# Performance work log

Hardware: AMD Instinct MI355X
Metric: run time of the kernel (lower is better)

Reference implementation:

```python
import jax, jax.numpy as jnp
import numpy as np

NEG_INF = 1e10  # module's self.inf


def setup_inputs() -> dict:
    key = jax.random.key(0)
    k1, k2, k3, k4 = jax.random.split(key, 4)
    B, To, Ti, d = 16, 2048, 2048, 64
    q = jax.random.normal(k1, (B, To, d), dtype=jnp.float32)
    k = jax.random.normal(k2, (B, Ti, d), dtype=jnp.float32)
    v = jax.random.normal(k3, (B, Ti, d), dtype=jnp.float32)
    prod_mask = jax.random.randint(k4, (B, To, Ti), 0, 2, dtype=jnp.int32)
    return {"q": q, "k": k, "v": v, "prod_mask": prod_mask}


def reference(q, k, v, prod_mask):
    d_qk = q.shape[2]
    # [B, To, Ti] scores
    scaled_qk = jnp.einsum('bod,bid->boi', q, k) / jnp.sqrt(jnp.float32(d_qk))
    scaled_qk = jnp.where(prod_mask == 0, jnp.float32(-NEG_INF), scaled_qk)
    weights = jax.nn.softmax(scaled_qk, axis=2)
    # v flattened over trailing dims is already [B, Ti, d] here
    attended_v = jnp.einsum('boi,bid->bod', weights, v)
    return attended_v
```

## Files before the change

kernel.cpp:

```cpp
#include <hip/hip_runtime.h>
#include <stdint.h>

#define BATCH 16
#define TO 2048
#define TI 2048
#define DH 64
#define NITER (TI / 64)

typedef __attribute__((ext_vector_type(8))) short bf16x8;
typedef __attribute__((ext_vector_type(4))) float f32x4;

__device__ __forceinline__ unsigned short f2bf(float f) {
  uint32_t x = __float_as_uint(f);
  x += 0x7fffu + ((x >> 16) & 1u);
  return (unsigned short)(x >> 16);
}

__global__ __launch_bounds__(256) void convert_kv(
    const float* __restrict__ kg, const float* __restrict__ vg,
    unsigned short* __restrict__ k_bf, unsigned short* __restrict__ v_t) {
  __shared__ __align__(16) unsigned short vt[64][72];
  int b = blockIdx.y;
  int i0 = blockIdx.x * 64;
  int t = threadIdx.x;

  {
    const float4* src = (const float4*)(kg + ((size_t)b * TI + i0) * DH);
    ushort4* dst = (ushort4*)(k_bf + ((size_t)b * TI + i0) * DH);
#pragma unroll
    for (int u = 0; u < 4; ++u) {
      float4 f = src[t + 256 * u];
      ushort4 o;
      o.x = f2bf(f.x); o.y = f2bf(f.y); o.z = f2bf(f.z); o.w = f2bf(f.w);
      dst[t + 256 * u] = o;
    }
  }
  {
    const float4* src = (const float4*)(vg + ((size_t)b * TI + i0) * DH);
#pragma unroll
    for (int u = 0; u < 4; ++u) {
      int idx = t + 256 * u;
      int row = idx >> 4;
      int c4 = idx & 15;
      float4 f = src[idx];
      vt[c4 * 4 + 0][row] = f2bf(f.x);
      vt[c4 * 4 + 1][row] = f2bf(f.y);
      vt[c4 * 4 + 2][row] = f2bf(f.z);
      vt[c4 * 4 + 3][row] = f2bf(f.w);
    }
  }
  __syncthreads();
  {
    int dd = t >> 2, part = t & 3;
    ushort4* dst = (ushort4*)(v_t + ((size_t)b * DH + dd) * TI + i0 + part * 16);
#pragma unroll
    for (int u = 0; u < 4; ++u) {
      ushort4 o;
      o.x = vt[dd][part * 16 + u * 4 + 0];
      o.y = vt[dd][part * 16 + u * 4 + 1];
      o.z = vt[dd][part * 16 + u * 4 + 2];
      o.w = vt[dd][part * 16 + u * 4 + 3];
      dst[u] = o;
    }
  }
}

#define ATTN_BODY(CUR, IC, MCUR, MNXT)                                         \
  {                                                                            \
    if ((IC) < NITER - 1) {                                                    \
      _Pragma("unroll") for (int mt = 0; mt < 4; ++mt)                         \
          MNXT[mt] = *(const int4*)(mbase + mt * 16);                          \
      mbase += 64;                                                             \
         \
      *(uint4*)&k_lds[(CUR) ^ 1][row][part * 16] = ka0;                        \
      *(uint4*)&k_lds[(CUR) ^ 1][row][part * 16 + 8] = ka1;                    \
      *(uint4*)&v_lds[(CUR) ^ 1][row][part * 16] = va0;                        \
      *(uint4*)&v_lds[(CUR) ^ 1][row][part * 16 + 8] = va1;                    \
    }                                                                          \
        \
    if ((IC) < NITER - 2) {                                                    \
      ka0 = kp[0]; ka1 = kp[1];                                                \
      va0 = vp[0]; va1 = vp[1];                                                \
      kp = (const uint4*)((const char*)kp + 64 * DH * 2);                      \
      vp = (const uint4*)((const char*)vp + 64 * 2);                           \
    }                                                                          \
                                                  \
    f32x4 st[4];                                                               \
    _Pragma("unroll") for (int mt = 0; mt < 4; ++mt) {                         \
      bf16x8 kf0 = *(const bf16x8*)&k_lds[CUR][mt * 16 + ln15][quad * 8];      \
      bf16x8 kf1 = *(const bf16x8*)&k_lds[CUR][mt * 16 + ln15][32 + quad * 8]; \
      f32x4 acc = (f32x4){0.f, 0.f, 0.f, 0.f};                                 \
      acc = __builtin_amdgcn_mfma_f32_16x16x32_bf16(kf0, qf[0], acc, 0, 0, 0); \
      acc = __builtin_amdgcn_mfma_f32_16x16x32_bf16(kf1, qf[1], acc, 0, 0, 0); \
      st[mt] = acc;                                                            \
    }                                                                          \
         \
    _Pragma("unroll") for (int mt = 0; mt < 4; ++mt) {                         \
      float p0 = (MCUR[mt].x != 0) ? __expf(st[mt][0]) : 0.f;                  \
      float p1 = (MCUR[mt].y != 0) ? __expf(st[mt][1]) : 0.f;                  \
      float p2 = (MCUR[mt].z != 0) ? __expf(st[mt][2]) : 0.f;                  \
      float p3 = (MCUR[mt].w != 0) ? __expf(st[mt][3]) : 0.f;                  \
      l_part += (p0 + p1) + (p2 + p3);                                         \
      uint32_t lo = (uint32_t)f2bf(p0) | ((uint32_t)f2bf(p1) << 16);           \
      uint32_t hi = (uint32_t)f2bf(p2) | ((uint32_t)f2bf(p3) << 16);           \
      uint2 pk; pk.x = lo; pk.y = hi;                                          \
      *(uint2*)&p_row[wave][ln15][mt * 16 + quad * 4] = pk;                    \
    }                                                                          \
            \
    bf16x8 pf0 = *(const bf16x8*)&p_row[wave][ln15][quad * 8];                 \
    bf16x8 pf1 = *(const bf16x8*)&p_row[wave][ln15][32 + quad * 8];            \
                                             \
    _Pragma("unroll") for (int dt = 0; dt < 4; ++dt) {                         \
      bf16x8 vf0 = *(const bf16x8*)&v_lds[CUR][dt * 16 + ln15][quad * 8];      \
      bf16x8 vf1 = *(const bf16x8*)&v_lds[CUR][dt * 16 + ln15][32 + quad * 8]; \
      o_acc[dt] = __builtin_amdgcn_mfma_f32_16x16x32_bf16(vf0, pf0, o_acc[dt], 0, 0, 0); \
      o_acc[dt] = __builtin_amdgcn_mfma_f32_16x16x32_bf16(vf1, pf1, o_acc[dt], 0, 0, 0); \
    }                                                                          \
          \
    asm volatile("s_waitcnt lgkmcnt(0)\n\ts_barrier" ::: "memory");            \
  }

__global__ __launch_bounds__(256) void attn_kernel(
    const float* __restrict__ q, const int* __restrict__ mask,
    const unsigned short* __restrict__ k_bf, const unsigned short* __restrict__ v_t,
    float* __restrict__ out) {
  __shared__ __align__(16) unsigned short k_lds[2][64][72];
  __shared__ __align__(16) unsigned short v_lds[2][64][72];
  __shared__ __align__(16) unsigned short p_row[4][16][72];

  int n = blockIdx.x;
  int xcd = n & 7;
  int slot = n >> 3;
  int b = (xcd << 1) | (slot >> 5);
  int o_blk = slot & 31;

  int t = threadIdx.x;
  int wave = t >> 6;
  int lane = t & 63;
  int ln15 = lane & 15;
  int quad = lane >> 4;

  int o0 = o_blk * 64 + wave * 16;
  int qrow = o0 + ln15;

  bf16x8 qf[2];
  {
    const float* qp = q + ((size_t)b * TO + qrow) * DH;
#pragma unroll
    for (int kc = 0; kc < 2; ++kc) {
      int kk = kc * 32 + quad * 8;
      float4 f0 = *(const float4*)(qp + kk);
      float4 f1 = *(const float4*)(qp + kk + 4);
      bf16x8 a;
      a[0] = (short)f2bf(f0.x * 0.125f);
      a[1] = (short)f2bf(f0.y * 0.125f);
      a[2] = (short)f2bf(f0.z * 0.125f);
      a[3] = (short)f2bf(f0.w * 0.125f);
      a[4] = (short)f2bf(f1.x * 0.125f);
      a[5] = (short)f2bf(f1.y * 0.125f);
      a[6] = (short)f2bf(f1.z * 0.125f);
      a[7] = (short)f2bf(f1.w * 0.125f);
      qf[kc] = a;
    }
  }

  f32x4 o_acc[4];
#pragma unroll
  for (int dt = 0; dt < 4; ++dt) o_acc[dt] = (f32x4){0.f, 0.f, 0.f, 0.f};
  float l_part = 0.f;

  int row = t >> 2, part = t & 3;
  const uint4* kp = (const uint4*)(k_bf + ((size_t)b * TI + row) * DH + part * 16);
  const uint4* vp = (const uint4*)(v_t + ((size_t)b * DH + row) * TI + part * 16);
  const int* mbase = mask + ((size_t)b * TO + qrow) * TI + quad * 4;

  uint4 ka0 = kp[0], ka1 = kp[1];
  uint4 va0 = vp[0], va1 = vp[1];
  kp = (const uint4*)((const char*)kp + 64 * DH * 2);
  vp = (const uint4*)((const char*)vp + 64 * 2);
  *(uint4*)&k_lds[0][row][part * 16] = ka0;
  *(uint4*)&k_lds[0][row][part * 16 + 8] = ka1;
  *(uint4*)&v_lds[0][row][part * 16] = va0;
  *(uint4*)&v_lds[0][row][part * 16 + 8] = va1;
  ka0 = kp[0]; ka1 = kp[1];
  va0 = vp[0]; va1 = vp[1];
  kp = (const uint4*)((const char*)kp + 64 * DH * 2);
  vp = (const uint4*)((const char*)vp + 64 * 2);
  int4 mv[4], mw[4];
#pragma unroll
  for (int mt = 0; mt < 4; ++mt) mv[mt] = *(const int4*)(mbase + mt * 16);
  mbase += 64;
  asm volatile("s_waitcnt lgkmcnt(0)\n\ts_barrier" ::: "memory");

  for (int ic = 0; ic < NITER; ic += 2) {
    ATTN_BODY(0, ic, mv, mw)
    ATTN_BODY(1, ic + 1, mw, mv)
  }

  l_part += __shfl_xor(l_part, 16);
  l_part += __shfl_xor(l_part, 32);
  float inv = 1.0f / l_part;
  float* orow = out + ((size_t)b * TO + qrow) * DH;
#pragma unroll
  for (int dt = 0; dt < 4; ++dt) {
    float4 vout;
    vout.x = o_acc[dt][0] * inv;
    vout.y = o_acc[dt][1] * inv;
    vout.z = o_acc[dt][2] * inv;
    vout.w = o_acc[dt][3] * inv;
    *(float4*)(orow + dt * 16 + quad * 4) = vout;
  }
}

extern "C" void kernel_launch(void* const* d_in, const int* in_sizes, int n_in,
                              void* d_out, int out_size, void* d_ws, size_t ws_size,
                              hipStream_t stream) {
  const float* q = (const float*)d_in[0];
  const float* k = (const float*)d_in[1];
  const float* v = (const float*)d_in[2];
  const int* mask = (const int*)d_in[3];

  unsigned short* k_bf = (unsigned short*)d_ws;
  unsigned short* v_t = k_bf + (size_t)BATCH * TI * DH;

  convert_kv<<<dim3(TI / 64, BATCH), 256, 0, stream>>>(k, v, k_bf, v_t);
  attn_kernel<<<dim3(TO / 64 * BATCH), 256, 0, stream>>>(q, mask, k_bf, v_t, (float*)d_out);
}
```

Measured before the change: 77.57 us.

## Load K and V MFMA fragments directly from global memory, drop LDS staging

```diff
diff --git a/kernel.cpp b/kernel.cpp
--- a/kernel.cpp
+++ b/kernel.cpp
@@ -65,33 +65,27 @@
   }
 }
 
-#define ATTN_BODY(CUR, IC, MCUR, MNXT)                                         \
+#define ATTN_BODY(IC, MCUR, MNXT)                                              \
   {                                                                            \
     if ((IC) < NITER - 1) {                                                    \
       _Pragma("unroll") for (int mt = 0; mt < 4; ++mt)                         \
           MNXT[mt] = *(const int4*)(mbase + mt * 16);                          \
       mbase += 64;                                                             \
-         \
-      *(uint4*)&k_lds[(CUR) ^ 1][row][part * 16] = ka0;                        \
-      *(uint4*)&k_lds[(CUR) ^ 1][row][part * 16 + 8] = ka1;                    \
-      *(uint4*)&v_lds[(CUR) ^ 1][row][part * 16] = va0;                        \
-      *(uint4*)&v_lds[(CUR) ^ 1][row][part * 16 + 8] = va1;                    \
-    }                                                                          \
-        \
-    if ((IC) < NITER - 2) {                                                    \
-      ka0 = kp[0]; ka1 = kp[1];                                                \
-      va0 = vp[0]; va1 = vp[1];                                                \
-      kp = (const uint4*)((const char*)kp + 64 * DH * 2);                      \
-      vp = (const uint4*)((const char*)vp + 64 * 2);                           \
-    }                                                                          \
-                                                  \
+    }                                                                          \
+                              \
+    const unsigned short* kc = k_base + (size_t)(IC) * 64 * DH;                \
+    bf16x8 kf[8];                                                              \
+    _Pragma("unroll") for (int mt = 0; mt < 4; ++mt) {                         \
+      const unsigned short* kr = kc + (mt * 16 + ln15) * DH + quad * 8;        \
+      kf[2 * mt] = *(const bf16x8*)kr;                                         \
+      kf[2 * mt + 1] = *(const bf16x8*)(kr + 32);                              \
+    }                                                                          \
+                                                              \
     f32x4 st[4];                                                               \
     _Pragma("unroll") for (int mt = 0; mt < 4; ++mt) {                         \
-      bf16x8 kf0 = *(const bf16x8*)&k_lds[CUR][mt * 16 + ln15][quad * 8];      \
-      bf16x8 kf1 = *(const bf16x8*)&k_lds[CUR][mt * 16 + ln15][32 + quad * 8]; \
       f32x4 acc = (f32x4){0.f, 0.f, 0.f, 0.f};                                 \
-      acc = __builtin_amdgcn_mfma_f32_16x16x32_bf16(kf0, qf[0], acc, 0, 0, 0); \
-      acc = __builtin_amdgcn_mfma_f32_16x16x32_bf16(kf1, qf[1], acc, 0, 0, 0); \
+      acc = __builtin_amdgcn_mfma_f32_16x16x32_bf16(kf[2 * mt], qf[0], acc, 0, 0, 0);     \
+      acc = __builtin_amdgcn_mfma_f32_16x16x32_bf16(kf[2 * mt + 1], qf[1], acc, 0, 0, 0); \
       st[mt] = acc;                                                            \
     }                                                                          \
          \
@@ -109,23 +103,21 @@
             \
     bf16x8 pf0 = *(const bf16x8*)&p_row[wave][ln15][quad * 8];                 \
     bf16x8 pf1 = *(const bf16x8*)&p_row[wave][ln15][32 + quad * 8];            \
-                                             \
+                     \
+    const unsigned short* vc = v_base + (size_t)(IC) * 64;                     \
     _Pragma("unroll") for (int dt = 0; dt < 4; ++dt) {                         \
-      bf16x8 vf0 = *(const bf16x8*)&v_lds[CUR][dt * 16 + ln15][quad * 8];      \
-      bf16x8 vf1 = *(const bf16x8*)&v_lds[CUR][dt * 16 + ln15][32 + quad * 8]; \
+      const unsigned short* vr = vc + (size_t)(dt * 16 + ln15) * TI + quad * 8;\
+      bf16x8 vf0 = *(const bf16x8*)vr;                                         \
+      bf16x8 vf1 = *(const bf16x8*)(vr + 32);                                  \
       o_acc[dt] = __builtin_amdgcn_mfma_f32_16x16x32_bf16(vf0, pf0, o_acc[dt], 0, 0, 0); \
       o_acc[dt] = __builtin_amdgcn_mfma_f32_16x16x32_bf16(vf1, pf1, o_acc[dt], 0, 0, 0); \
     }                                                                          \
-          \
-    asm volatile("s_waitcnt lgkmcnt(0)\n\ts_barrier" ::: "memory");            \
   }
 
 __global__ __launch_bounds__(256) void attn_kernel(
     const float* __restrict__ q, const int* __restrict__ mask,
     const unsigned short* __restrict__ k_bf, const unsigned short* __restrict__ v_t,
     float* __restrict__ out) {
-  __shared__ __align__(16) unsigned short k_lds[2][64][72];
-  __shared__ __align__(16) unsigned short v_lds[2][64][72];
   __shared__ __align__(16) unsigned short p_row[4][16][72];
 
   int n = blockIdx.x;
@@ -169,32 +161,18 @@
   for (int dt = 0; dt < 4; ++dt) o_acc[dt] = (f32x4){0.f, 0.f, 0.f, 0.f};
   float l_part = 0.f;
 
-  int row = t >> 2, part = t & 3;
-  const uint4* kp = (const uint4*)(k_bf + ((size_t)b * TI + row) * DH + part * 16);
-  const uint4* vp = (const uint4*)(v_t + ((size_t)b * DH + row) * TI + part * 16);
+  const unsigned short* k_base = k_bf + (size_t)b * TI * DH;
+  const unsigned short* v_base = v_t + (size_t)b * DH * TI;
   const int* mbase = mask + ((size_t)b * TO + qrow) * TI + quad * 4;
 
-  uint4 ka0 = kp[0], ka1 = kp[1];
-  uint4 va0 = vp[0], va1 = vp[1];
-  kp = (const uint4*)((const char*)kp + 64 * DH * 2);
-  vp = (const uint4*)((const char*)vp + 64 * 2);
-  *(uint4*)&k_lds[0][row][part * 16] = ka0;
-  *(uint4*)&k_lds[0][row][part * 16 + 8] = ka1;
-  *(uint4*)&v_lds[0][row][part * 16] = va0;
-  *(uint4*)&v_lds[0][row][part * 16 + 8] = va1;
-  ka0 = kp[0]; ka1 = kp[1];
-  va0 = vp[0]; va1 = vp[1];
-  kp = (const uint4*)((const char*)kp + 64 * DH * 2);
-  vp = (const uint4*)((const char*)vp + 64 * 2);
   int4 mv[4], mw[4];
 #pragma unroll
   for (int mt = 0; mt < 4; ++mt) mv[mt] = *(const int4*)(mbase + mt * 16);
   mbase += 64;
-  asm volatile("s_waitcnt lgkmcnt(0)\n\ts_barrier" ::: "memory");
 
   for (int ic = 0; ic < NITER; ic += 2) {
-    ATTN_BODY(0, ic, mv, mw)
-    ATTN_BODY(1, ic + 1, mw, mv)
+    ATTN_BODY(ic, mv, mw)
+    ATTN_BODY(ic + 1, mw, mv)
   }
 
   l_part += __shfl_xor(l_part, 16);
```

Result: slower. 159.9 us (+106.1%).

## Split key dimension across two wave groups per block with LDS reduction

Applied to the files above, without the earlier changes.

```diff
diff --git a/kernel.cpp b/kernel.cpp
--- a/kernel.cpp
+++ b/kernel.cpp
@@ -5,7 +5,7 @@
 #define TO 2048
 #define TI 2048
 #define DH 64
-#define NITER (TI / 64)
+#define NITER2 16
 
 typedef __attribute__((ext_vector_type(8))) short bf16x8;
 typedef __attribute__((ext_vector_type(4))) float f32x4;
@@ -65,30 +65,18 @@
   }
 }
 
-#define ATTN_BODY(CUR, IC, MCUR, MNXT)                                         \
+#define ATTN_BODY(IC, MCUR, MNXT)                                              \
   {                                                                            \
-    if ((IC) < NITER - 1) {                                                    \
+    if ((IC) < NITER2 - 1) {                                                   \
       _Pragma("unroll") for (int mt = 0; mt < 4; ++mt)                         \
           MNXT[mt] = *(const int4*)(mbase + mt * 16);                          \
       mbase += 64;                                                             \
-         \
-      *(uint4*)&k_lds[(CUR) ^ 1][row][part * 16] = ka0;                        \
-      *(uint4*)&k_lds[(CUR) ^ 1][row][part * 16 + 8] = ka1;                    \
-      *(uint4*)&v_lds[(CUR) ^ 1][row][part * 16] = va0;                        \
-      *(uint4*)&v_lds[(CUR) ^ 1][row][part * 16 + 8] = va1;                    \
-    }                                                                          \
-        \
-    if ((IC) < NITER - 2) {                                                    \
-      ka0 = kp[0]; ka1 = kp[1];                                                \
-      va0 = vp[0]; va1 = vp[1];                                                \
-      kp = (const uint4*)((const char*)kp + 64 * DH * 2);                      \
-      vp = (const uint4*)((const char*)vp + 64 * 2);                           \
-    }                                                                          \
-                                                  \
+    }                                                                          \
+                                        \
     f32x4 st[4];                                                               \
     _Pragma("unroll") for (int mt = 0; mt < 4; ++mt) {                         \
-      bf16x8 kf0 = *(const bf16x8*)&k_lds[CUR][mt * 16 + ln15][quad * 8];      \
-      bf16x8 kf1 = *(const bf16x8*)&k_lds[CUR][mt * 16 + ln15][32 + quad * 8]; \
+      bf16x8 kf0 = *(const bf16x8*)&k_lds[g][mt * 16 + ln15][quad * 8];        \
+      bf16x8 kf1 = *(const bf16x8*)&k_lds[g][mt * 16 + ln15][32 + quad * 8];   \
       f32x4 acc = (f32x4){0.f, 0.f, 0.f, 0.f};                                 \
       acc = __builtin_amdgcn_mfma_f32_16x16x32_bf16(kf0, qf[0], acc, 0, 0, 0); \
       acc = __builtin_amdgcn_mfma_f32_16x16x32_bf16(kf1, qf[1], acc, 0, 0, 0); \
@@ -109,24 +97,40 @@
             \
     bf16x8 pf0 = *(const bf16x8*)&p_row[wave][ln15][quad * 8];                 \
     bf16x8 pf1 = *(const bf16x8*)&p_row[wave][ln15][32 + quad * 8];            \
-                                             \
+                                                         \
     _Pragma("unroll") for (int dt = 0; dt < 4; ++dt) {                         \
-      bf16x8 vf0 = *(const bf16x8*)&v_lds[CUR][dt * 16 + ln15][quad * 8];      \
-      bf16x8 vf1 = *(const bf16x8*)&v_lds[CUR][dt * 16 + ln15][32 + quad * 8]; \
+      bf16x8 vf0 = *(const bf16x8*)&v_lds[g][dt * 16 + ln15][quad * 8];        \
+      bf16x8 vf1 = *(const bf16x8*)&v_lds[g][dt * 16 + ln15][32 + quad * 8];   \
       o_acc[dt] = __builtin_amdgcn_mfma_f32_16x16x32_bf16(vf0, pf0, o_acc[dt], 0, 0, 0); \
       o_acc[dt] = __builtin_amdgcn_mfma_f32_16x16x32_bf16(vf1, pf1, o_acc[dt], 0, 0, 0); \
     }                                                                          \
-          \
+                                          \
     asm volatile("s_waitcnt lgkmcnt(0)\n\ts_barrier" ::: "memory");            \
-  }
-
-__global__ __launch_bounds__(256) void attn_kernel(
+    if ((IC) < NITER2 - 1) {                                                   \
+                        \
+      *(uint4*)&k_lds[g][row][part * 16] = ka0;                                \
+      *(uint4*)&k_lds[g][row][part * 16 + 8] = ka1;                            \
+      *(uint4*)&v_lds[g][row][part * 16] = va0;                                \
+      *(uint4*)&v_lds[g][row][part * 16 + 8] = va1;                            \
+               \
+      if ((IC) < NITER2 - 2) {                                                 \
+        ka0 = kp[0]; ka1 = kp[1];                                              \
+        va0 = vp[0]; va1 = vp[1];                                              \
+        kp = (const uint4*)((const char*)kp + 64 * DH * 2);                    \
+        vp = (const uint4*)((const char*)vp + 64 * 2);                         \
+      }                                                                        \
+                                    \
+      asm volatile("s_waitcnt lgkmcnt(0)\n\ts_barrier" ::: "memory");          \
+    }                                                                          \
+  }
+
+__global__ __launch_bounds__(512) void attn_kernel(
     const float* __restrict__ q, const int* __restrict__ mask,
     const unsigned short* __restrict__ k_bf, const unsigned short* __restrict__ v_t,
     float* __restrict__ out) {
   __shared__ __align__(16) unsigned short k_lds[2][64][72];
   __shared__ __align__(16) unsigned short v_lds[2][64][72];
-  __shared__ __align__(16) unsigned short p_row[4][16][72];
+  __shared__ __align__(16) unsigned short p_row[8][16][72];
 
   int n = blockIdx.x;
   int xcd = n & 7;
@@ -136,12 +140,13 @@
 
   int t = threadIdx.x;
   int wave = t >> 6;
+  int g = wave >> 2;
+  int w = wave & 3;
   int lane = t & 63;
   int ln15 = lane & 15;
   int quad = lane >> 4;
 
-  int o0 = o_blk * 64 + wave * 16;
-  int qrow = o0 + ln15;
+  int qrow = o_blk * 64 + w * 16 + ln15;
 
   bf16x8 qf[2];
   {
@@ -169,19 +174,20 @@
   for (int dt = 0; dt < 4; ++dt) o_acc[dt] = (f32x4){0.f, 0.f, 0.f, 0.f};
   float l_part = 0.f;
 
-  int row = t >> 2, part = t & 3;
-  const uint4* kp = (const uint4*)(k_bf + ((size_t)b * TI + row) * DH + part * 16);
-  const uint4* vp = (const uint4*)(v_t + ((size_t)b * DH + row) * TI + part * 16);
-  const int* mbase = mask + ((size_t)b * TO + qrow) * TI + quad * 4;
+  int tg = t & 255;
+  int row = tg >> 2, part = tg & 3;
+  const uint4* kp = (const uint4*)(k_bf + ((size_t)b * TI + g * 1024 + row) * DH + part * 16);
+  const uint4* vp = (const uint4*)(v_t + ((size_t)b * DH + row) * TI + g * 1024 + part * 16);
+  const int* mbase = mask + ((size_t)b * TO + qrow) * TI + g * 1024 + quad * 4;
 
   uint4 ka0 = kp[0], ka1 = kp[1];
   uint4 va0 = vp[0], va1 = vp[1];
   kp = (const uint4*)((const char*)kp + 64 * DH * 2);
   vp = (const uint4*)((const char*)vp + 64 * 2);
-  *(uint4*)&k_lds[0][row][part * 16] = ka0;
-  *(uint4*)&k_lds[0][row][part * 16 + 8] = ka1;
-  *(uint4*)&v_lds[0][row][part * 16] = va0;
-  *(uint4*)&v_lds[0][row][part * 16 + 8] = va1;
+  *(uint4*)&k_lds[g][row][part * 16] = ka0;
+  *(uint4*)&k_lds[g][row][part * 16 + 8] = ka1;
+  *(uint4*)&v_lds[g][row][part * 16] = va0;
+  *(uint4*)&v_lds[g][row][part * 16 + 8] = va1;
   ka0 = kp[0]; ka1 = kp[1];
   va0 = vp[0]; va1 = vp[1];
   kp = (const uint4*)((const char*)kp + 64 * DH * 2);
@@ -192,23 +198,38 @@
   mbase += 64;
   asm volatile("s_waitcnt lgkmcnt(0)\n\ts_barrier" ::: "memory");
 
-  for (int ic = 0; ic < NITER; ic += 2) {
-    ATTN_BODY(0, ic, mv, mw)
-    ATTN_BODY(1, ic + 1, mw, mv)
+  for (int ic = 0; ic < NITER2; ic += 2) {
+    ATTN_BODY(ic, mv, mw)
+    ATTN_BODY(ic + 1, mw, mv)
   }
 
   l_part += __shfl_xor(l_part, 16);
   l_part += __shfl_xor(l_part, 32);
-  float inv = 1.0f / l_part;
-  float* orow = out + ((size_t)b * TO + qrow) * DH;
-#pragma unroll
-  for (int dt = 0; dt < 4; ++dt) {
-    float4 vout;
-    vout.x = o_acc[dt][0] * inv;
-    vout.y = o_acc[dt][1] * inv;
-    vout.z = o_acc[dt][2] * inv;
-    vout.w = o_acc[dt][3] * inv;
-    *(float4*)(orow + dt * 16 + quad * 4) = vout;
+
+  float* scr = (float*)&k_lds[0][0][0];
+  float* lscr = (float*)&p_row[0][0][0];
+  int orow_i = w * 16 + ln15;
+
+  if (g == 1) {
+#pragma unroll
+    for (int dt = 0; dt < 4; ++dt)
+      *(f32x4*)&scr[(size_t)orow_i * 68 + dt * 16 + quad * 4] = o_acc[dt];
+    if (quad == 0) lscr[orow_i] = l_part;
+  }
+  asm volatile("s_waitcnt lgkmcnt(0)\n\ts_barrier" ::: "memory");
+  if (g == 0) {
+    float inv = 1.0f / (l_part + lscr[orow_i]);
+    float* orow = out + ((size_t)b * TO + qrow) * DH;
+#pragma unroll
+    for (int dt = 0; dt < 4; ++dt) {
+      f32x4 other = *(const f32x4*)&scr[(size_t)orow_i * 68 + dt * 16 + quad * 4];
+      float4 vout;
+      vout.x = (o_acc[dt][0] + other[0]) * inv;
+      vout.y = (o_acc[dt][1] + other[1]) * inv;
+      vout.z = (o_acc[dt][2] + other[2]) * inv;
+      vout.w = (o_acc[dt][3] + other[3]) * inv;
+      *(float4*)(orow + dt * 16 + quad * 4) = vout;
+    }
   }
 }
 
@@ -224,5 +245,5 @@
   unsigned short* v_t = k_bf + (size_t)BATCH * TI * DH;
 
   convert_kv<<<dim3(TI / 64, BATCH), 256, 0, stream>>>(k, v, k_bf, v_t);
-  attn_kernel<<<dim3(TO / 64 * BATCH), 256, 0, stream>>>(q, mask, k_bf, v_t, (float*)d_out);
-}
+  attn_kernel<<<dim3(TO / 64 * BATCH), 512, 0, stream>>>(q, mask, k_bf, v_t, (float*)d_out);
+}
```

Result: slower. 90.86 us (+17.1%).
